# Performance work log

Measured on AMD Instinct MI355X. Metric: run time of the kernel, lower is better.

Reference implementation:

```python
import jax, jax.numpy as jnp
import numpy as np
import math

EMB_S = 64
HEADS = 8
EMB = EMB_S * HEADS  # 512
M = int(EMB_S * 0.5)  # 32 random features
B, T = 8, 4096
EPS = 1e-5


def setup_inputs() -> dict:
    key = jax.random.key(0)
    ks = jax.random.split(key, 16)
    s_in = 1.0 / math.sqrt(EMB_S)
    s_emb = 1.0 / math.sqrt(EMB)
    s_hid = 1.0 / math.sqrt(4 * EMB)
    return {
        "x": jax.random.normal(ks[0], (B, T, EMB), jnp.float32),
        "w": jax.random.normal(ks[1], (M, EMB_S), jnp.float32),  # frozen random features
        "kqv_w": jax.random.uniform(ks[2], (3 * EMB_S, EMB_S), jnp.float32, -s_in, s_in),
        "kqv_b": jax.random.uniform(ks[3], (3 * EMB_S,), jnp.float32, -s_in, s_in),
        "proj_w": jax.random.uniform(ks[4], (EMB, EMB), jnp.float32, -s_emb, s_emb),
        "proj_b": jax.random.uniform(ks[5], (EMB,), jnp.float32, -s_emb, s_emb),
        "ln1_g": 1.0 + 0.02 * jax.random.normal(ks[6], (EMB,), jnp.float32),
        "ln1_b": 0.02 * jax.random.normal(ks[7], (EMB,), jnp.float32),
        "ln2_g": 1.0 + 0.02 * jax.random.normal(ks[8], (EMB,), jnp.float32),
        "ln2_b": 0.02 * jax.random.normal(ks[9], (EMB,), jnp.float32),
        "mlp_w1": jax.random.uniform(ks[10], (4 * EMB, EMB), jnp.float32, -s_emb, s_emb),
        "mlp_b1": jax.random.uniform(ks[11], (4 * EMB,), jnp.float32, -s_emb, s_emb),
        "mlp_w2": jax.random.uniform(ks[12], (EMB, 4 * EMB), jnp.float32, -s_hid, s_hid),
        "mlp_b2": jax.random.uniform(ks[13], (EMB,), jnp.float32, -s_hid, s_hid),
    }


def _layer_norm(x, g, b):
    mu = jnp.mean(x, axis=-1, keepdims=True)
    var = jnp.mean(jnp.square(x - mu), axis=-1, keepdims=True)
    return (x - mu) * jax.lax.rsqrt(var + EPS) * g + b


def _prm_exp(z, w):
    # z: [B,T,H,E]; softmax-kernel random features, [B,T,H,M]
    xd = 0.5 * jnp.sum(z * z, axis=-1, keepdims=True)
    wtx = jnp.einsum("bthe,me->bthm", z, w)
    return jnp.exp(wtx - xd) / math.sqrt(M)


def reference(x, w, kqv_w, kqv_b, proj_w, proj_b, ln1_g, ln1_b, ln2_g, ln2_b,
              mlp_w1, mlp_b1, mlp_w2, mlp_b2):
    Bb, Tt, _ = x.shape
    h = _layer_norm(x, ln1_g, ln1_b).reshape(Bb, Tt, HEADS, EMB_S)
    kqv = jnp.einsum("bthe,fe->bthf", h, kqv_w) + kqv_b  # [B,T,H,3E]
    k, q, v = jnp.split(kqv, 3, axis=-1)  # torch.split order: k, q, v
    kp = _prm_exp(k, w)  # [B,T,H,M]
    qp = _prm_exp(q, w)
    D = jnp.einsum("bthm,bhm->bth", qp, kp.sum(axis=1))  # [B,T,H]
    kptv = jnp.einsum("bthe,bthm->bhem", v, kp)  # [B,H,E,M]
    y = jnp.einsum("bthm,bhem->bthe", qp, kptv) / D[..., None]
    y = y.reshape(Bb, Tt, EMB)
    attn = jnp.einsum("btf,ef->bte", y, proj_w) + proj_b  # dropout = identity (eval)
    x = x + attn
    h2 = _layer_norm(x, ln2_g, ln2_b)
    hid = jax.nn.gelu(jnp.einsum("bte,fe->btf", h2, mlp_w1) + mlp_b1, approximate=False)
    mlp_out = jnp.einsum("btf,ef->bte", hid, mlp_w2) + mlp_b2
    return x + mlp_out
```

## Files before the change

kernel.cpp:

```cpp
#include <hip/hip_runtime.h>
#include <hip/hip_bf16.h>

typedef __bf16 bf16x8_t __attribute__((ext_vector_type(8)));
typedef float f32x4_t __attribute__((ext_vector_type(4)));
using bf16 = __hip_bfloat16;

#define EMB 512
#define NTOK 32768
#define NROW 262144
#define SQRT_M_INV 0.17677669529663687f

__device__ __forceinline__ void gload16(const void* g, void* l) {
  __builtin_amdgcn_global_load_lds((const __attribute__((address_space(1))) void*)g,
                                   (__attribute__((address_space(3))) void*)l, 16, 0, 0);
}

__device__ __forceinline__ void cvt4(const float* __restrict__ in,
                                     bf16* __restrict__ out, int i4, int n4) {
  if (i4 < n4) {
    float4 v = ((const float4*)in)[i4];
    alignas(8) bf16 o[4];
    o[0] = __float2bfloat16(v.x); o[1] = __float2bfloat16(v.y);
    o[2] = __float2bfloat16(v.z); o[3] = __float2bfloat16(v.w);
    *(uint2*)(out + i4 * 4) = *(const uint2*)o;
  }
}
__global__ __launch_bounds__(256) void f2b4_kernel(
    const float* __restrict__ a, bf16* __restrict__ oa, int na4,
    const float* __restrict__ b, bf16* __restrict__ ob, int nb4,
    const float* __restrict__ c, bf16* __restrict__ oc, int nc4,
    const float* __restrict__ d, bf16* __restrict__ od, int nd4) {
  int i4 = blockIdx.x * 256 + threadIdx.x;
  cvt4(a, oa, i4, na4);
  cvt4(b, ob, i4, nb4);
  cvt4(c, oc, i4, nc4);
  cvt4(d, od, i4, nd4);
}

__global__ __launch_bounds__(256) void ln_kernel(const float* __restrict__ x,
                                                 const float* __restrict__ g,
                                                 const float* __restrict__ bt,
                                                 bf16* __restrict__ out) {
  int lane = threadIdx.x & 63;
  int row = blockIdx.x * 4 + (threadIdx.x >> 6);
  const float* xr = x + (size_t)row * EMB;
  float4 v0 = ((const float4*)xr)[lane * 2];
  float4 v1 = ((const float4*)xr)[lane * 2 + 1];
  float s = v0.x + v0.y + v0.z + v0.w + v1.x + v1.y + v1.z + v1.w;
#pragma unroll
  for (int o = 32; o; o >>= 1) s += __shfl_xor(s, o);
  float mu = s * (1.0f / 512.0f);
  float vs = 0.f, d;
  d = v0.x - mu; vs += d * d;  d = v0.y - mu; vs += d * d;
  d = v0.z - mu; vs += d * d;  d = v0.w - mu; vs += d * d;
  d = v1.x - mu; vs += d * d;  d = v1.y - mu; vs += d * d;
  d = v1.z - mu; vs += d * d;  d = v1.w - mu; vs += d * d;
#pragma unroll
  for (int o = 32; o; o >>= 1) vs += __shfl_xor(vs, o);
  float rstd = rsqrtf(vs * (1.0f / 512.0f) + 1e-5f);
  float4 g0 = ((const float4*)g)[lane * 2], g1 = ((const float4*)g)[lane * 2 + 1];
  float4 b0 = ((const float4*)bt)[lane * 2], b1 = ((const float4*)bt)[lane * 2 + 1];
  alignas(16) bf16 o8[8];
  o8[0] = __float2bfloat16((v0.x - mu) * rstd * g0.x + b0.x);
  o8[1] = __float2bfloat16((v0.y - mu) * rstd * g0.y + b0.y);
  o8[2] = __float2bfloat16((v0.z - mu) * rstd * g0.z + b0.z);
  o8[3] = __float2bfloat16((v0.w - mu) * rstd * g0.w + b0.w);
  o8[4] = __float2bfloat16((v1.x - mu) * rstd * g1.x + b1.x);
  o8[5] = __float2bfloat16((v1.y - mu) * rstd * g1.y + b1.y);
  o8[6] = __float2bfloat16((v1.z - mu) * rstd * g1.z + b1.z);
  o8[7] = __float2bfloat16((v1.w - mu) * rstd * g1.w + b1.w);
  *(uint4*)(out + (size_t)row * EMB + lane * 8) = *(const uint4*)o8;
}

template <int BM, int BN, int WM, int WN, int OP>
__global__ __launch_bounds__(256) void gemm_bt(const bf16* __restrict__ A,
                                               const bf16* __restrict__ W,
                                               const float* __restrict__ bias,
                                               const float* __restrict__ res,
                                               float* __restrict__ outF,
                                               bf16* __restrict__ outB,
                                               int M, int N, int K) {
  constexpr int BK = 32;
  constexpr int TM = BM / WM, TN = BN / WN;
  constexpr int NI = TM / 16, NJ = TN / 16;
  alignas(16) __shared__ bf16 As[BM * BK];
  alignas(16) __shared__ bf16 Ws[BN * BK];
  int t = threadIdx.x;
  int lane = t & 63, wid = t >> 6;
  int wm = wid % WM, wn = wid / WM;
  int bn = blockIdx.x * BN, bm = blockIdx.y * BM;
  int lr = lane & 15, lq = lane >> 4;
  const int r0 = (t * 8) >> 5, c0 = (t * 8) & 31;

  f32x4_t acc[NI][NJ];
#pragma unroll
  for (int i = 0; i < NI; ++i)
#pragma unroll
    for (int j = 0; j < NJ; ++j)
#pragma unroll
      for (int r = 0; r < 4; ++r) acc[i][j][r] = 0.f;

  for (int k0 = 0; k0 < K; k0 += BK) {
#pragma unroll
    for (int p = 0; p < BM * BK / 2048; ++p) {
      int r = r0 + p * 64;
      gload16(&A[(size_t)(bm + r) * K + k0 + c0], &As[r * BK + c0]);
    }
#pragma unroll
    for (int p = 0; p < BN * BK / 2048; ++p) {
      int r = r0 + p * 64;
      gload16(&W[(size_t)(bn + r) * K + k0 + c0], &Ws[r * BK + c0]);
    }
    __syncthreads();
    bf16x8_t afr[NI], bfr[NJ];
#pragma unroll
    for (int i = 0; i < NI; ++i)
      afr[i] = *(const bf16x8_t*)&As[(wm * TM + i * 16 + lr) * BK + lq * 8];
#pragma unroll
    for (int j = 0; j < NJ; ++j)
      bfr[j] = *(const bf16x8_t*)&Ws[(wn * TN + j * 16 + lr) * BK + lq * 8];
#pragma unroll
    for (int i = 0; i < NI; ++i)
#pragma unroll
      for (int j = 0; j < NJ; ++j)
        acc[i][j] = __builtin_amdgcn_mfma_f32_16x16x32_bf16(afr[i], bfr[j], acc[i][j], 0, 0, 0);
    __syncthreads();
  }

#pragma unroll
  for (int i = 0; i < NI; ++i)
#pragma unroll
    for (int j = 0; j < NJ; ++j) {
      int gn = bn + wn * TN + j * 16 + lr;
      float bv = bias[gn];
#pragma unroll
      for (int r = 0; r < 4; ++r) {
        int gm = bm + wm * TM + i * 16 + lq * 4 + r;
        float v = acc[i][j][r] + bv;
        size_t off = (size_t)gm * N + gn;
        if (OP == 0) {
          outF[off] = v;
        } else if (OP == 1) {
          outF[off] = v + res[off];
        } else {
          float gg = 0.5f * v * (1.0f + erff(v * 0.70710678118654752f));
          outB[off] = __float2bfloat16(gg);
        }
      }
    }
}

__device__ __forceinline__ size_t bh_row(size_t grow) {
  size_t h = grow & 7, bt = grow >> 3;
  size_t b = bt >> 12, tt = bt & 4095;
  return ((b * 8 + h) << 12) + tt;
}

__global__ __launch_bounds__(256) void kqv_prm_kernel(
    const bf16* __restrict__ A,
    const bf16* __restrict__ Wk,
    const float* __restrict__ bias,
    const float* __restrict__ wrf,
    float* __restrict__ kp, float* __restrict__ qp,
    bf16* __restrict__ vout) {
  constexpr int LDZ = 136;
  constexpr int LDV = 72;
  alignas(16) __shared__ char u_raw[27648];
  bf16* As  = (bf16*)u_raw;
  bf16* Ws  = (bf16*)(u_raw + 4096);
  bf16* zkq = (bf16*)u_raw;
  bf16* vs  = (bf16*)(u_raw + 17408);
  float* xd_s = (float*)(u_raw + 26624);

  int t = threadIdx.x;
  int lane = t & 63, wid = t >> 6;
  int wm = wid & 1, wn = wid >> 1;
  int lr = lane & 15, lq = lane >> 4;
  size_t row0 = (size_t)blockIdx.x * 64;

  bf16x8_t wfrag[2][2];
#pragma unroll
  for (int mt = 0; mt < 2; ++mt)
#pragma unroll
    for (int ks = 0; ks < 2; ++ks) {
      const float* src = wrf + (mt * 16 + lr) * 64 + ks * 32 + lq * 8;
#pragma unroll
      for (int jj = 0; jj < 8; ++jj) wfrag[mt][ks][jj] = (__bf16)src[jj];
    }

  f32x4_t acc[2][6];
#pragma unroll
  for (int i = 0; i < 2; ++i)
#pragma unroll
    for (int j = 0; j < 6; ++j)
#pragma unroll
      for (int r = 0; r < 4; ++r) acc[i][j][r] = 0.f;

  const int r0 = t >> 2, c0 = (t * 8) & 31;
  for (int k0 = 0; k0 < 64; k0 += 32) {
    gload16(&A[(row0 + r0) * 64 + k0 + c0], &As[r0 * 32 + c0]);
#pragma unroll
    for (int p = 0; p < 3; ++p) {
      int r = r0 + p * 64;
      gload16(&Wk[(size_t)r * 64 + k0 + c0], &Ws[r * 32 + c0]);
    }
    __syncthreads();
    bf16x8_t af[2], bfr[6];
#pragma unroll
    for (int i = 0; i < 2; ++i)
      af[i] = *(const bf16x8_t*)&As[(wm * 32 + i * 16 + lr) * 32 + lq * 8];
#pragma unroll
    for (int j = 0; j < 6; ++j)
      bfr[j] = *(const bf16x8_t*)&Ws[(wn * 96 + j * 16 + lr) * 32 + lq * 8];
#pragma unroll
    for (int i = 0; i < 2; ++i)
#pragma unroll
      for (int j = 0; j < 6; ++j)
        acc[i][j] = __builtin_amdgcn_mfma_f32_16x16x32_bf16(af[i], bfr[j], acc[i][j], 0, 0, 0);
    __syncthreads();
  }

#pragma unroll
  for (int i = 0; i < 2; ++i)
#pragma unroll
    for (int j = 0; j < 6; ++j) {
      int col = wn * 96 + j * 16 + lr;
      float bv = bias[col];
      int rowb = wm * 32 + i * 16 + lq * 4;
#pragma unroll
      for (int r = 0; r < 4; ++r) {
        float v = acc[i][j][r] + bv;
        if (col < 128) zkq[(rowb + r) * LDZ + col] = __float2bfloat16(v);
        else           vs[(rowb + r) * LDV + (col - 128)] = __float2bfloat16(v);
      }
    }
  __syncthreads();

  if (t < 128) {
    int r = t & 63, sel = t >> 6;
    const bf16* zr = &zkq[r * LDZ + sel * 64];
    float xd = 0.f;
#pragma unroll
    for (int c = 0; c < 64; c += 8) {
      bf16x8_t z8 = *(const bf16x8_t*)&zr[c];
#pragma unroll
      for (int jj = 0; jj < 8; ++jj) { float f = (float)z8[jj]; xd += f * f; }
    }
    xd_s[r * 2 + sel] = 0.5f * xd;
  }
  __syncthreads();

#pragma unroll
  for (int p = 0; p < 2; ++p) {
    int idx = t + p * 256;
    int r = idx >> 3, c8 = idx & 7;
    size_t nr = bh_row(row0 + r);
    *(uint4*)&vout[nr * 64 + c8 * 8] = *(const uint4*)&vs[r * LDV + c8 * 8];
  }

  int sel = wn;
  f32x4_t aw[2][2];
#pragma unroll
  for (int i = 0; i < 2; ++i)
#pragma unroll
    for (int mt = 0; mt < 2; ++mt)
#pragma unroll
      for (int r = 0; r < 4; ++r) aw[i][mt][r] = 0.f;
#pragma unroll
  for (int ks = 0; ks < 2; ++ks) {
    bf16x8_t af2[2];
#pragma unroll
    for (int i = 0; i < 2; ++i)
      af2[i] = *(const bf16x8_t*)&zkq[(wm * 32 + i * 16 + lr) * LDZ + sel * 64 + ks * 32 + lq * 8];
#pragma unroll
    for (int i = 0; i < 2; ++i)
#pragma unroll
      for (int mt = 0; mt < 2; ++mt)
        aw[i][mt] = __builtin_amdgcn_mfma_f32_16x16x32_bf16(af2[i], wfrag[mt][ks], aw[i][mt], 0, 0, 0);
  }
  float* outp = sel ? qp : kp;
#pragma unroll
  for (int i = 0; i < 2; ++i)
#pragma unroll
    for (int r = 0; r < 4; ++r) {
      int row = wm * 32 + i * 16 + lq * 4 + r;
      size_t nr = bh_row(row0 + row);
#pragma unroll
      for (int mt = 0; mt < 2; ++mt) {
        int m = mt * 16 + lr;
        outp[nr * 32 + m] =
            __expf(aw[i][mt][r] - xd_s[row * 2 + sel]) * SQRT_M_INV;
      }
    }
}

__global__ __launch_bounds__(256) void kptv_kernel(const bf16* __restrict__ v2,
                                                   const float* __restrict__ kp2,
                                                   float* __restrict__ part) {
  int bh = blockIdx.x, chunk = blockIdx.y;
  int t = threadIdx.x, e = t & 63, g = t >> 6;
  const bf16* vp = v2 + ((size_t)bh * 4096 + chunk * 512) * 64 + e;
  const float* kpp = kp2 + ((size_t)bh * 4096 + chunk * 512) * 32 + g * 8;
  float acc[8] = {0.f, 0.f, 0.f, 0.f, 0.f, 0.f, 0.f, 0.f};
  float accs[8] = {0.f, 0.f, 0.f, 0.f, 0.f, 0.f, 0.f, 0.f};
#pragma unroll 8
  for (int tok = 0; tok < 512; ++tok) {
    float vv = __bfloat162float(vp[tok * 64]);
    float4 k0 = *(const float4*)(kpp + tok * 32);
    float4 k1 = *(const float4*)(kpp + tok * 32 + 4);
    acc[0] += vv * k0.x; acc[1] += vv * k0.y; acc[2] += vv * k0.z; acc[3] += vv * k0.w;
    acc[4] += vv * k1.x; acc[5] += vv * k1.y; acc[6] += vv * k1.z; acc[7] += vv * k1.w;
    accs[0] += k0.x; accs[1] += k0.y; accs[2] += k0.z; accs[3] += k0.w;
    accs[4] += k1.x; accs[5] += k1.y; accs[6] += k1.z; accs[7] += k1.w;
  }
  float* pp = part + (size_t)(bh * 8 + chunk) * 2080 + e * 32 + g * 8;
  *(float4*)pp = make_float4(acc[0], acc[1], acc[2], acc[3]);
  *(float4*)(pp + 4) = make_float4(acc[4], acc[5], acc[6], acc[7]);
  if (e == 0) {
    float* ps = part + (size_t)(bh * 8 + chunk) * 2080 + 2048 + g * 8;
    *(float4*)ps = make_float4(accs[0], accs[1], accs[2], accs[3]);
    *(float4*)(ps + 4) = make_float4(accs[4], accs[5], accs[6], accs[7]);
  }
}

__global__ __launch_bounds__(256) void y_kernel(const float* __restrict__ qp2,
                                                const float* __restrict__ part,
                                                bf16* __restrict__ y) {
  int bh = blockIdx.x, chunk = blockIdx.y;
  int b = bh >> 3, h = bh & 7;
  alignas(16) __shared__ float qp_s[16][32];
  int t = threadIdx.x;
  int e = t & 63, iq = t >> 6;
  float kv[32], ks[32];
#pragma unroll
  for (int m = 0; m < 32; ++m) { kv[m] = 0.f; ks[m] = 0.f; }
  for (int c = 0; c < 8; ++c) {
    const float* pp = part + (size_t)(bh * 8 + c) * 2080;
#pragma unroll
    for (int m = 0; m < 32; m += 4) {
      float4 a = *(const float4*)&pp[e * 32 + m];
      kv[m] += a.x; kv[m + 1] += a.y; kv[m + 2] += a.z; kv[m + 3] += a.w;
      float4 s = *(const float4*)&pp[2048 + m];
      ks[m] += s.x; ks[m + 1] += s.y; ks[m + 2] += s.z; ks[m + 3] += s.w;
    }
  }
  for (int grp = 0; grp < 32; ++grp) {
    int tok0 = chunk * 512 + grp * 16;
    __syncthreads();
    if (t < 128) {
      int r = t >> 3, c4 = t & 7;
      *(float4*)&qp_s[r][c4 * 4] =
          *(const float4*)(qp2 + ((size_t)bh * 4096 + tok0 + r) * 32 + c4 * 4);
    }
    __syncthreads();
#pragma unroll
    for (int i0 = 0; i0 < 4; ++i0) {
      int i = iq * 4 + i0;
      float dot = 0.f, dd = 0.f;
#pragma unroll
      for (int m = 0; m < 32; m += 4) {
        float4 qq = *(const float4*)&qp_s[i][m];
        dot += qq.x * kv[m] + qq.y * kv[m + 1] + qq.z * kv[m + 2] + qq.w * kv[m + 3];
        dd  += qq.x * ks[m] + qq.y * ks[m + 1] + qq.z * ks[m + 2] + qq.w * ks[m + 3];
      }
      y[(size_t)(b * 4096 + tok0 + i) * EMB + h * 64 + e] = __float2bfloat16(dot / dd);
    }
  }
}

extern "C" void kernel_launch(void* const* d_in, const int* in_sizes, int n_in,
                              void* d_out, int out_size, void* d_ws, size_t ws_size,
                              hipStream_t stream) {
  const float* x      = (const float*)d_in[0];
  const float* w      = (const float*)d_in[1];
  const float* kqv_w  = (const float*)d_in[2];
  const float* kqv_b  = (const float*)d_in[3];
  const float* proj_w = (const float*)d_in[4];
  const float* proj_b = (const float*)d_in[5];
  const float* ln1_g  = (const float*)d_in[6];
  const float* ln1_b  = (const float*)d_in[7];
  const float* ln2_g  = (const float*)d_in[8];
  const float* ln2_b  = (const float*)d_in[9];
  const float* mlp_w1 = (const float*)d_in[10];
  const float* mlp_b1 = (const float*)d_in[11];
  const float* mlp_w2 = (const float*)d_in[12];
  const float* mlp_b2 = (const float*)d_in[13];
  float* out = (float*)d_out;

  char* ws = (char*)d_ws;
  size_t off = 0;
  auto alloc = [&](size_t bytes) -> void* {
    void* p = ws + off;
    off = (off + bytes + 255) & ~(size_t)255;
    return p;
  };

  bf16* kqv_wb  = (bf16*)alloc(12288 * 2);
  bf16* proj_wb = (bf16*)alloc(262144 * 2);
  bf16* w1b     = (bf16*)alloc(1048576 * 2);
  bf16* w2b     = (bf16*)alloc(1048576 * 2);
  bf16* hb      = (bf16*)alloc((size_t)NTOK * EMB * 2);
  bf16* yb      = hb;
  float* qpb    = (float*)alloc((size_t)NROW * 32 * 4);
  bf16* h2b     = (bf16*)qpb;
  float* kpb    = (float*)alloc((size_t)NROW * 32 * 4);
  bf16* hidb    = (bf16*)kpb;
  bf16* vb      = (bf16*)alloc((size_t)NROW * 64 * 2);
  float* partb  = (float*)alloc((size_t)512 * 2080 * 4);

  f2b4_kernel<<<1024, 256, 0, stream>>>(kqv_w, kqv_wb, 12288 / 4,
                                        proj_w, proj_wb, 262144 / 4,
                                        mlp_w1, w1b, 1048576 / 4,
                                        mlp_w2, w2b, 1048576 / 4);

  ln_kernel<<<NTOK / 4, 256, 0, stream>>>(x, ln1_g, ln1_b, hb);

  kqv_prm_kernel<<<NROW / 64, 256, 0, stream>>>(hb, kqv_wb, kqv_b, w, kpb, qpb, vb);

  kptv_kernel<<<dim3(64, 8), 256, 0, stream>>>(vb, kpb, partb);

  y_kernel<<<dim3(64, 8), 256, 0, stream>>>(qpb, partb, yb);

  gemm_bt<128, 128, 2, 2, 1><<<dim3(4, NTOK / 128), 256, 0, stream>>>(
      yb, proj_wb, proj_b, x, out, nullptr, NTOK, 512, 512);

  ln_kernel<<<NTOK / 4, 256, 0, stream>>>(out, ln2_g, ln2_b, h2b);

  for (int c = 0; c < 2; ++c) {
    const bf16* h2c = h2b + (size_t)c * 16384 * 512;
    float* outc = out + (size_t)c * 16384 * 512;
    gemm_bt<128, 128, 2, 2, 2><<<dim3(16, 128), 256, 0, stream>>>(
        h2c, w1b, mlp_b1, nullptr, nullptr, hidb, 16384, 2048, 512);
    gemm_bt<128, 128, 2, 2, 1><<<dim3(4, 128), 256, 0, stream>>>(
        hidb, w2b, mlp_b2, outc, outc, nullptr, 16384, 512, 2048);
  }
}
```

Before: 664.0 us.

## Double-buffer GEMM LDS tiles and use polynomial erf approximation for GELU

The bf16 GEMM now keeps two LDS buffers and issues the global-to-LDS loads for the next K tile before computing the current one. This replaces the load-sync-compute-sync pattern with a single barrier per iteration, aiming to overlap memory latency with MFMA work. The exact erff in the GELU epilogue is also swapped for the Abramowitz-Stegun polynomial built on rcp and exp. That cuts epilogue ALU cost but adds small approximation error and doubles the shared memory each block uses, which may lower occupancy.

New measurement: 641.6 us. 3.4% less time.

```diff
diff --git a/kernel.cpp b/kernel.cpp
--- a/kernel.cpp
+++ b/kernel.cpp
@@ -13,6 +13,21 @@
 __device__ __forceinline__ void gload16(const void* g, void* l) {
   __builtin_amdgcn_global_load_lds((const __attribute__((address_space(1))) void*)g,
                                    (__attribute__((address_space(3))) void*)l, 16, 0, 0);
+}
+
+__device__ __forceinline__ float fast_gelu(float v) {
+  float u = v * 0.70710678118654752f;
+  float a = fabsf(u);
+  float tt = __builtin_amdgcn_rcpf(fmaf(0.3275911f, a, 1.0f));
+  float p = fmaf(tt, 1.061405429f, -1.453152027f);
+  p = fmaf(tt, p, 1.421413741f);
+  p = fmaf(tt, p, -0.284496736f);
+  p = fmaf(tt, p, 0.254829592f);
+  p = p * tt;
+  float e = __expf(-a * a);
+  float er = fmaf(-p, e, 1.0f);
+  er = copysignf(er, u);
+  return 0.5f * v * (1.0f + er);
 }
 
 __device__ __forceinline__ void cvt4(const float* __restrict__ in,
@@ -83,8 +98,10 @@
   constexpr int BK = 32;
   constexpr int TM = BM / WM, TN = BN / WN;
   constexpr int NI = TM / 16, NJ = TN / 16;
-  alignas(16) __shared__ bf16 As[BM * BK];
-  alignas(16) __shared__ bf16 Ws[BN * BK];
+  constexpr int AP = BM * BK / 2048;
+  constexpr int WP = BN * BK / 2048;
+  alignas(16) __shared__ bf16 As[2][BM * BK];
+  alignas(16) __shared__ bf16 Ws[2][BN * BK];
   int t = threadIdx.x;
   int lane = t & 63, wid = t >> 6;
   int wm = wid % WM, wn = wid / WM;
@@ -92,6 +109,10 @@
   int lr = lane & 15, lq = lane >> 4;
   const int r0 = (t * 8) >> 5, c0 = (t * 8) & 31;
 
+  const bf16* ap = A + (size_t)(bm + r0) * K + c0;
+  const bf16* wp = W + (size_t)(bn + r0) * K + c0;
+  const size_t strA = (size_t)64 * K;
+
   f32x4_t acc[NI][NJ];
 #pragma unroll
   for (int i = 0; i < NI; ++i)
@@ -100,32 +121,42 @@
 #pragma unroll
       for (int r = 0; r < 4; ++r) acc[i][j][r] = 0.f;
 
-  for (int k0 = 0; k0 < K; k0 += BK) {
-#pragma unroll
-    for (int p = 0; p < BM * BK / 2048; ++p) {
-      int r = r0 + p * 64;
-      gload16(&A[(size_t)(bm + r) * K + k0 + c0], &As[r * BK + c0]);
-    }
-#pragma unroll
-    for (int p = 0; p < BN * BK / 2048; ++p) {
-      int r = r0 + p * 64;
-      gload16(&W[(size_t)(bn + r) * K + k0 + c0], &Ws[r * BK + c0]);
-    }
-    __syncthreads();
+  auto stage = [&](int buf) {
+#pragma unroll
+    for (int p = 0; p < AP; ++p)
+      gload16(ap + (size_t)p * strA, &As[buf][(r0 + p * 64) * BK + c0]);
+#pragma unroll
+    for (int p = 0; p < WP; ++p)
+      gload16(wp + (size_t)p * strA, &Ws[buf][(r0 + p * 64) * BK + c0]);
+    ap += BK;
+    wp += BK;
+  };
+  auto compute = [&](int buf) {
     bf16x8_t afr[NI], bfr[NJ];
 #pragma unroll
     for (int i = 0; i < NI; ++i)
-      afr[i] = *(const bf16x8_t*)&As[(wm * TM + i * 16 + lr) * BK + lq * 8];
+      afr[i] = *(const bf16x8_t*)&As[buf][(wm * TM + i * 16 + lr) * BK + lq * 8];
 #pragma unroll
     for (int j = 0; j < NJ; ++j)
-      bfr[j] = *(const bf16x8_t*)&Ws[(wn * TN + j * 16 + lr) * BK + lq * 8];
+      bfr[j] = *(const bf16x8_t*)&Ws[buf][(wn * TN + j * 16 + lr) * BK + lq * 8];
 #pragma unroll
     for (int i = 0; i < NI; ++i)
 #pragma unroll
       for (int j = 0; j < NJ; ++j)
         acc[i][j] = __builtin_amdgcn_mfma_f32_16x16x32_bf16(afr[i], bfr[j], acc[i][j], 0, 0, 0);
+  };
+
+  const int nt = K / BK;
+  stage(0);
+  int cur = 0;
+  for (int kt = 0; kt < nt - 1; ++kt) {
     __syncthreads();
-  }
+    stage(cur ^ 1);
+    compute(cur);
+    cur ^= 1;
+  }
+  __syncthreads();
+  compute(cur);
 
 #pragma unroll
   for (int i = 0; i < NI; ++i)
@@ -143,8 +174,7 @@
         } else if (OP == 1) {
           outF[off] = v + res[off];
         } else {
-          float gg = 0.5f * v * (1.0f + erff(v * 0.70710678118654752f));
-          outB[off] = __float2bfloat16(gg);
+          outB[off] = __float2bfloat16(fast_gelu(v));
         }
       }
     }
```
